# Kernel tuning notes

Measured on AMD Instinct MI355X. Metric: run time of the kernel, lower is better.

The kernel has to match this reference:

```python
import jax, jax.numpy as jnp
import numpy as np

B, S, D, H = 2, 2048, 1024, 16
HD = D // H  # 64
EPS = 1e-6


def setup_inputs() -> dict:
    key = jax.random.key(0)
    ks = jax.random.split(key, 12)
    s = 1.0 / np.sqrt(D)
    return {
        "query": jax.random.normal(ks[0], (B, S, D), jnp.float32),
        "key": jax.random.normal(ks[1], (B, S, D), jnp.float32),
        "value": jax.random.normal(ks[2], (B, S, D), jnp.float32),
        "mask": jax.random.randint(ks[3], (B, S, S), 0, 2) == 1,
        "Wq": jax.random.normal(ks[4], (D, D), jnp.float32) * s,
        "bq": jnp.zeros((D,), jnp.float32),
        "Wk": jax.random.normal(ks[5], (D, D), jnp.float32) * s,
        "bk": jnp.zeros((D,), jnp.float32),
        "Wv": jax.random.normal(ks[6], (D, D), jnp.float32) * s,
        "bv": jnp.zeros((D,), jnp.float32),
        "Wo": jax.random.normal(ks[7], (D, D), jnp.float32) * s,
        "bo": jnp.zeros((D,), jnp.float32),
        "gamma": jnp.ones((D,), jnp.float32),
        "beta": jnp.zeros((D,), jnp.float32),
    }


def reference(query, key, value, mask, Wq, bq, Wk, bk, Wv, bv, Wo, bo, gamma, beta):
    b, sq, _ = query.shape
    sk = key.shape[1]
    # QKV projections -> [b, h, s, hd]
    q = (query @ Wq + bq).reshape(b, sq, H, HD).transpose(0, 2, 1, 3)
    k = (key @ Wk + bk).reshape(b, sk, H, HD).transpose(0, 2, 1, 3)
    v = (value @ Wv + bv).reshape(b, sk, H, HD).transpose(0, 2, 1, 3)
    # scores [b, h, sq, sk]
    scores = jnp.einsum("bhqd,bhkd->bhqk", q, k) / jnp.sqrt(jnp.float32(HD))
    scores = jnp.where(mask[:, None, :, :], -jnp.inf, scores)
    attn = jax.nn.softmax(scores, axis=-1)  # dropout: eval mode (identity)
    out = jnp.einsum("bhqk,bhkd->bhqd", attn, v)
    out = out.transpose(0, 2, 1, 3).reshape(b, sq, H * HD)
    out = out @ Wo + bo
    # residual + LayerNorm with unbiased std and (std + eps) denominator (faithful to torch code)
    x = query + out
    mean = x.mean(-1, keepdims=True)
    std = jnp.std(x, axis=-1, keepdims=True, ddof=1)
    return gamma * (x - mean) / (std + EPS) + beta
```

## Files before the change

### kernel.cpp

```cpp
#include <hip/hip_runtime.h>


#define NB 2
#define SS 2048
#define DDIM 1024
#define NH 16
#define HDIM 64
#define MROWS (NB * SS)

typedef unsigned short u16;
typedef unsigned long long u64;
typedef unsigned int u32;
typedef short bf16x8 __attribute__((ext_vector_type(8)));
typedef float f32x4 __attribute__((ext_vector_type(4)));

typedef const __attribute__((address_space(1))) void GASV;
typedef __attribute__((address_space(3))) void LASV;

__device__ __forceinline__ float dev_exp2(float x) {
  float r;
  asm("v_exp_f32 %0, %1" : "=v"(r) : "v"(x));
  return r;
}

__device__ __forceinline__ u16 f2bf(float f) {
  unsigned u = __builtin_bit_cast(unsigned, f);
  u += 0x7FFFu + ((u >> 16) & 1u);
  return (u16)(u >> 16);
}

__device__ __forceinline__ u32 cvt_pk_bf16(float a, float b) {
  u32 d;
  asm("v_cvt_pk_bf16_f32 %0, %1, %2" : "=v"(d) : "v"(a), "v"(b));
  return d;
}

__global__ __launch_bounds__(256) void cvt_bf16_3(const float* __restrict__ q,
                                                  const float* __restrict__ k,
                                                  const float* __restrict__ v,
                                                  u16* __restrict__ out) {
  const float* in = (blockIdx.y == 0) ? q : (blockIdx.y == 1) ? k : v;
  size_t i = ((size_t)blockIdx.x * 256 + threadIdx.x) * 4;
  float4 val = *(const float4*)(in + i);
  uint2 o;
  u16* po = (u16*)&o;
  po[0] = f2bf(val.x); po[1] = f2bf(val.y); po[2] = f2bf(val.z); po[3] = f2bf(val.w);
  *(uint2*)(out + (size_t)blockIdx.y * MROWS * DDIM + i) = o;
}

__global__ __launch_bounds__(256) void cvt_mask_bits(const int* __restrict__ in,
                                                     u64* __restrict__ out) {
  size_t w = ((size_t)blockIdx.x * 256 + threadIdx.x) >> 6;
  int lane = threadIdx.x & 63;
  int v = in[w * 64 + lane];
  u64 bits = __ballot(v != 0);
  if (lane == 0) out[w] = bits;
}

__global__ __launch_bounds__(256) void transpose_cvt_w4(const float* __restrict__ W0,
                                                        const float* __restrict__ W1,
                                                        const float* __restrict__ W2,
                                                        const float* __restrict__ W3,
                                                        u16* __restrict__ WTbase) {
  __shared__ u16 t[64][65];
  const int z = blockIdx.z;
  const float* W = (z == 0) ? W0 : (z == 1) ? W1 : (z == 2) ? W2 : W3;
  u16* WT = WTbase + (size_t)z * DDIM * DDIM;
  const int k0 = blockIdx.x * 64, n0 = blockIdx.y * 64;
  const int tid = threadIdx.x;
  const int r = tid >> 4;
  const int c4 = (tid & 15) * 4;
#pragma unroll
  for (int it = 0; it < 4; ++it) {
    int k = r + it * 16;
    float4 v = *(const float4*)&W[(size_t)(k0 + k) * DDIM + n0 + c4];
    t[c4 + 0][k] = f2bf(v.x);
    t[c4 + 1][k] = f2bf(v.y);
    t[c4 + 2][k] = f2bf(v.z);
    t[c4 + 3][k] = f2bf(v.w);
  }
  __syncthreads();
#pragma unroll
  for (int it = 0; it < 4; ++it) {
    int n = r + it * 16;
    uint2 o;
    u16* po = (u16*)&o;
#pragma unroll
    for (int j = 0; j < 4; ++j) po[j] = t[n][c4 + j];
    *(uint2*)&WT[(size_t)(n0 + n) * DDIM + k0 + c4] = o;
  }
}

template <int MODE>
__global__ __launch_bounds__(256) void gemm_bt(const u16* __restrict__ Abase,
                                               const u16* __restrict__ BT,
                                               const float* __restrict__ b0,
                                               const float* __restrict__ b1,
                                               const float* __restrict__ b2,
                                               const float* __restrict__ resid,
                                               void* __restrict__ C,
                                               void* __restrict__ Cv) {
  __shared__ __align__(16) u16 SMEM[2][2][128][64];
  u16(&Al)[2][128][64] = SMEM[0];
  u16(&Bl)[2][128][64] = SMEM[1];
  const int tid = threadIdx.x;
  const int wid = tid >> 6, lane = tid & 63;
  const int wm = (wid >> 1) * 64, wn = (wid & 1) * 64;
  const int nwg = gridDim.x * gridDim.y;
  const int lin = blockIdx.y * 32 + blockIdx.x;
  const int wg = (lin & 7) * (nwg >> 3) + (lin >> 3);
  const int rowA0 = (wg & 31) * 128, colB0 = (wg >> 5) * 128;
  const int sel = (MODE == 0) ? (colB0 >> 10) : 0;
  const u16* Ag = Abase + (size_t)sel * ((size_t)MROWS * DDIM) + (size_t)rowA0 * DDIM;
  const u16* Bg = BT + (size_t)colB0 * DDIM;
  f32x4 acc[4][4] = {};
  const int rl = lane >> 3;
  const int ce = (lane & 7) * 8;

#define G_STAGE(buf, kt)                                                       \
  do {                                                                         \
    _Pragma("unroll") for (int c = 0; c < 4; ++c) {                            \
      int rt = wid * 32 + c * 8;                                               \
      __builtin_amdgcn_global_load_lds(                                        \
          (GASV*)(Ag + (size_t)(rt + rl) * DDIM + (kt) + ce),                  \
          (LASV*)((char*)&Al[buf][0][0] + rt * 128), 16, 0, 0);                \
      __builtin_amdgcn_global_load_lds(                                        \
          (GASV*)(Bg + (size_t)(rt + rl) * DDIM + (kt) + ce),                  \
          (LASV*)((char*)&Bl[buf][0][0] + rt * 128), 16, 0, 0);                \
    }                                                                          \
  } while (0)

  G_STAGE(0, 0);
  __syncthreads();
  for (int t = 0; t < 16; ++t) {
    const int cur = t & 1;
    if (t < 15) G_STAGE(cur ^ 1, (t + 1) * 64);
#pragma unroll
    for (int kk = 0; kk < 64; kk += 32) {
      bf16x8 af[4], bfr[4];
#pragma unroll
      for (int i = 0; i < 4; ++i)
        af[i] = *(const bf16x8*)&Al[cur][wm + i * 16 + (lane & 15)][kk + (lane >> 4) * 8];
#pragma unroll
      for (int j = 0; j < 4; ++j)
        bfr[j] = *(const bf16x8*)&Bl[cur][wn + j * 16 + (lane & 15)][kk + (lane >> 4) * 8];
#pragma unroll
      for (int i = 0; i < 4; ++i)
#pragma unroll
        for (int j = 0; j < 4; ++j)
          acc[i][j] = __builtin_amdgcn_mfma_f32_16x16x32_bf16(af[i], bfr[j], acc[i][j], 0, 0, 0);
    }
    __syncthreads();
  }
#undef G_STAGE

  const int cb = lane & 15, hi = lane >> 4;
  if (MODE == 0) {
    if (sel == 2) {
      u16(*T)[136] = (u16(*)[136]) & SMEM[0][0][0][0];
      const int dcol0 = colB0 & 1023;
#pragma unroll
      for (int j = 0; j < 4; ++j) {
        int dl = wn + j * 16 + cb;
        float bv = b2[dcol0 + dl];
#pragma unroll
        for (int i = 0; i < 4; ++i) {
          int sl = wm + i * 16 + hi * 4;
          uint2 o;
          o.x = cvt_pk_bf16(acc[i][j][0] + bv, acc[i][j][1] + bv);
          o.y = cvt_pk_bf16(acc[i][j][2] + bv, acc[i][j][3] + bv);
          *(uint2*)&T[dl][sl] = o;
        }
      }
      __syncthreads();
      const int bb = rowA0 >> 11, s0 = rowA0 & (SS - 1);
#pragma unroll
      for (int it = 0; it < 8; ++it) {
        int chunk = it * 256 + tid;
        int dl = chunk >> 4;
        int sc = (chunk & 15) * 8;
        int dg = dcol0 + dl;
        *(bf16x8*)&((u16*)Cv)[((size_t)(bb * NH + (dg >> 6)) * HDIM + (dg & 63)) * SS +
                              s0 + sc] = *(const bf16x8*)&T[dl][sc];
      }
    } else {
      const float* bp = (sel == 0) ? b0 : b1;
      const float scale = (sel == 0) ? 0.125f * 1.44269504088896340736f : 1.0f;
      u16* dst = (u16*)C + (size_t)sel * ((size_t)MROWS * DDIM);
      const int colw0 = (colB0 & 1023) + wn;
#pragma unroll
      for (int i = 0; i < 4; ++i)
#pragma unroll
        for (int j = 0; j < 4; ++j) {
          int colw = colw0 + j * 16 + cb;
          float bv = bp[colw];
#pragma unroll
          for (int r = 0; r < 4; ++r) {
            int row = rowA0 + wm + i * 16 + hi * 4 + r;
            dst[(size_t)row * DDIM + colw] = f2bf((acc[i][j][r] + bv) * scale);
          }
        }
    }
  } else {
#pragma unroll
    for (int i = 0; i < 4; ++i)
#pragma unroll
      for (int j = 0; j < 4; ++j) {
        int col = colB0 + wn + j * 16 + cb;
        float bv = b0[col];
#pragma unroll
        for (int r = 0; r < 4; ++r) {
          int row = rowA0 + wm + i * 16 + hi * 4 + r;
          size_t off = (size_t)row * DDIM + col;
          ((float*)C)[off] = acc[i][j][r] + bv + resid[off];
        }
      }
  }
}

__global__ __launch_bounds__(256, 4) void attn_fwd(const u16* __restrict__ Qp,
                                                   const u16* __restrict__ Kp,
                                                   const u16* __restrict__ VpT,
                                                   const u64* __restrict__ Mbits,
                                                   u16* __restrict__ O) {
  __shared__ __align__(16) u16 Kl[2][64][64];
  __shared__ __align__(16) u16 Vl[2][64][64];
  __shared__ __align__(16) u16 Pl[4][16][64];
  const int tid = threadIdx.x, wid = tid >> 6, lane = tid & 63;
  const int bid = blockIdx.x;
  const int bh = (bid & 7) * 4 + ((bid >> 3) & 3);
  const int q0 = (bid >> 5) * 64;
  const int b = bh >> 4, h = bh & 15;
  const int hi = lane >> 4, cbase = lane & 15, lx = lane & 7;

  bf16x8 qf[2];
  {
    const u16* qb = Qp + (size_t)(b * SS + q0 + wid * 16 + cbase) * DDIM + h * 64 + hi * 8;
    qf[0] = *(const bf16x8*)qb;
    qf[1] = *(const bf16x8*)(qb + 32);
  }
  const bf16x8 ONES8 = {(short)0x3F80, (short)0x3F80, (short)0x3F80, (short)0x3F80,
                        (short)0x3F80, (short)0x3F80, (short)0x3F80, (short)0x3F80};
  f32x4 l_acc = (f32x4){0.f, 0.f, 0.f, 0.f};
  f32x4 accO[4];
#pragma unroll
  for (int f = 0; f < 4; ++f) accO[f] = (f32x4){0.f, 0.f, 0.f, 0.f};

  const u16* Kgb = Kp + (size_t)b * SS * DDIM + h * 64;
  const u16* Vgb = VpT + (size_t)bh * 64 * SS;
  const u64* Mb = Mbits + (size_t)(b * SS + q0 + wid * 16 + cbase) * (SS / 64);
  const int rl = lane >> 3;
  const int ceS = ((lane & 7) ^ rl) * 8;

  int fo[4][2];
#pragma unroll
  for (int f = 0; f < 4; ++f)
#pragma unroll
    for (int ks = 0; ks < 2; ++ks)
      fo[f][ks] = (f * 16 + cbase) * 64 + (((ks * 4 + hi) ^ lx) << 3);
  int pw[4];
#pragma unroll
  for (int f = 0; f < 4; ++f)
    pw[f] = cbase * 64 + (((f * 2 + (hi >> 1)) ^ lx) << 3) + ((hi & 1) << 2);
  u16* KlF = &Kl[0][0][0];
  u16* VlF = &Vl[0][0][0];
  u16* Plw = &Pl[wid][0][0];

#define STAGE_KV(BUF, kv)                                                      \
  do {                                                                         \
    _Pragma("unroll") for (int c = 0; c < 2; ++c) {                            \
      int rt = wid * 16 + c * 8;                                               \
      __builtin_amdgcn_global_load_lds(                                        \
          (GASV*)(Kgb + (size_t)((kv) + rt + rl) * DDIM + ceS),                \
          (LASV*)((char*)KlF + (BUF) * 8192 + rt * 128), 16, 0, 0);            \
      __builtin_amdgcn_global_load_lds(                                        \
          (GASV*)(Vgb + (size_t)(rt + rl) * SS + (kv) + ceS),                  \
          (LASV*)((char*)VlF + (BUF) * 8192 + rt * 128), 16, 0, 0);            \
    }                                                                          \
  } while (0)

#define ATTN_ITER(T, CUR, DO_STAGE, MROW)                                      \
  do {                                                                         \
    if (DO_STAGE) STAGE_KV((CUR) ^ 1, ((T) + 1) * 64);                         \
    f32x4 sc[4];                                                               \
    __builtin_amdgcn_s_setprio(1);                                             \
    _Pragma("unroll") for (int fn = 0; fn < 4; ++fn) {                         \
      f32x4 c = (f32x4){0.f, 0.f, 0.f, 0.f};                                   \
      _Pragma("unroll") for (int ks = 0; ks < 2; ++ks) {                       \
        bf16x8 kf = *(const bf16x8*)(KlF + (CUR) * 4096 + fo[fn][ks]);         \
        c = __builtin_amdgcn_mfma_f32_16x16x32_bf16(kf, qf[ks], c, 0, 0, 0);   \
      }                                                                        \
      sc[fn] = c;                                                              \
    }                                                                          \
    __builtin_amdgcn_s_setprio(0);                                             \
             \
    u64 mh = (MROW) >> (hi * 4);                                               \
    u32 mlo = (u32)mh, mhi2 = (u32)(mh >> 32);                                 \
    _Pragma("unroll") for (int fn = 0; fn < 4; ++fn) {                         \
      u32 b4 = ((fn < 2) ? mlo : mhi2) >> ((fn & 1) * 16);                     \
      _Pragma("unroll") for (int j = 0; j < 4; ++j) {                          \
        float bf_ = (float)((b4 >> j) & 1u);                                   \
        sc[fn][j] = dev_exp2(fmaf(bf_, -512.f, sc[fn][j]));                    \
      }                                                                        \
    }                                                                          \
    _Pragma("unroll") for (int fn = 0; fn < 4; ++fn) {                         \
      uint2 wpair;                                                             \
      wpair.x = cvt_pk_bf16(sc[fn][0], sc[fn][1]);                             \
      wpair.y = cvt_pk_bf16(sc[fn][2], sc[fn][3]);                             \
      *(uint2*)(Plw + pw[fn]) = wpair;                                         \
    }                                                                          \
    bf16x8 pf0 = *(const bf16x8*)(Plw + fo[0][0]);                             \
    bf16x8 pf1 = *(const bf16x8*)(Plw + fo[0][1]);                             \
    __builtin_amdgcn_s_setprio(1);                                             \
    l_acc = __builtin_amdgcn_mfma_f32_16x16x32_bf16(pf0, ONES8, l_acc, 0, 0, 0); \
    l_acc = __builtin_amdgcn_mfma_f32_16x16x32_bf16(pf1, ONES8, l_acc, 0, 0, 0); \
    _Pragma("unroll") for (int nd = 0; nd < 4; ++nd) {                         \
      bf16x8 v0 = *(const bf16x8*)(VlF + (CUR) * 4096 + fo[nd][0]);            \
      bf16x8 v1 = *(const bf16x8*)(VlF + (CUR) * 4096 + fo[nd][1]);            \
      accO[nd] = __builtin_amdgcn_mfma_f32_16x16x32_bf16(pf0, v0, accO[nd], 0, 0, 0); \
      accO[nd] = __builtin_amdgcn_mfma_f32_16x16x32_bf16(pf1, v1, accO[nd], 0, 0, 0); \
    }                                                                          \
    __builtin_amdgcn_s_setprio(0);                                             \
    __syncthreads();                                                           \
  } while (0)

  STAGE_KV(0, 0);
  __syncthreads();
  for (int th = 0; th < 16; ++th) {
    uint4 mw = *(const uint4*)&Mb[2 * th];
    u64 m0 = ((u64)mw.y << 32) | mw.x;
    u64 m1 = ((u64)mw.w << 32) | mw.z;
    ATTN_ITER(2 * th, 0, true, m0);
    ATTN_ITER(2 * th + 1, 1, (th != 15), m1);
  }
#undef ATTN_ITER
#undef STAGE_KV

#pragma unroll
  for (int nd = 0; nd < 4; ++nd)
#pragma unroll
    for (int j = 0; j < 4; ++j) {
      int row = q0 + wid * 16 + hi * 4 + j;
      int col = h * 64 + nd * 16 + cbase;
      O[(size_t)(b * SS + row) * DDIM + col] = f2bf(accO[nd][j] / l_acc[j]);
    }
}

__global__ __launch_bounds__(256) void ln_res(const float* __restrict__ xin,
                                              const float* __restrict__ gamma,
                                              const float* __restrict__ beta,
                                              float* __restrict__ out) {
  const int row = blockIdx.x, tid = threadIdx.x;
  const size_t base = (size_t)row * DDIM + tid * 4;
  float4 x = *(const float4*)(xin + base);
  float x0 = x.x, x1 = x.y, x2 = x.z, x3 = x.w;
  float s = x0 + x1 + x2 + x3;
  __shared__ float red[4];
#pragma unroll
  for (int off = 32; off >= 1; off >>= 1) s += __shfl_xor(s, off, 64);
  const int wid = tid >> 6, lane = tid & 63;
  if (lane == 0) red[wid] = s;
  __syncthreads();
  float mean = (red[0] + red[1] + red[2] + red[3]) * (1.0f / DDIM);
  float d0 = x0 - mean, d1 = x1 - mean, d2 = x2 - mean, d3 = x3 - mean;
  float ss = d0 * d0 + d1 * d1 + d2 * d2 + d3 * d3;
#pragma unroll
  for (int off = 32; off >= 1; off >>= 1) ss += __shfl_xor(ss, off, 64);
  __syncthreads();
  if (lane == 0) red[wid] = ss;
  __syncthreads();
  float var = (red[0] + red[1] + red[2] + red[3]) * (1.0f / (DDIM - 1));
  float denom = sqrtf(var) + 1e-6f;
  float4 g = *(const float4*)(gamma + (size_t)tid * 4);
  float4 be = *(const float4*)(beta + (size_t)tid * 4);
  float4 o;
  o.x = g.x * d0 / denom + be.x;
  o.y = g.y * d1 / denom + be.y;
  o.z = g.z * d2 / denom + be.z;
  o.w = g.w * d3 / denom + be.w;
  *(float4*)(out + base) = o;
}

extern "C" void kernel_launch(void* const* d_in, const int* in_sizes, int n_in,
                              void* d_out, int out_size, void* d_ws, size_t ws_size,
                              hipStream_t stream) {
  const float* query = (const float*)d_in[0];
  const float* key = (const float*)d_in[1];
  const float* value = (const float*)d_in[2];
  const int* mask = (const int*)d_in[3];
  const float* Wq = (const float*)d_in[4];
  const float* bq = (const float*)d_in[5];
  const float* Wk = (const float*)d_in[6];
  const float* bk = (const float*)d_in[7];
  const float* Wv = (const float*)d_in[8];
  const float* bv = (const float*)d_in[9];
  const float* Wo = (const float*)d_in[10];
  const float* bo = (const float*)d_in[11];
  const float* gamma = (const float*)d_in[12];
  const float* beta = (const float*)d_in[13];
  float* out = (float*)d_out;
  char* ws = (char*)d_ws;
  const size_t MB = 1ull << 20;
  u16* qkvb = (u16*)(ws + 0 * MB);
  u16* WT = (u16*)(ws + 24 * MB);
  u16* WoT = (u16*)(ws + 30 * MB);
  u16* Qp = (u16*)(ws + 32 * MB);
  u16* Kp = (u16*)(ws + 40 * MB);
  u16* VpT = (u16*)(ws + 48 * MB);
  u16* attnb = (u16*)(ws + 56 * MB);
  u64* maskbits = (u64*)(ws + 0 * MB);
  float* proj = (float*)(ws + 8 * MB);

  cvt_bf16_3<<<dim3(MROWS * DDIM / 1024, 3), 256, 0, stream>>>(query, key, value, qkvb);
  transpose_cvt_w4<<<dim3(16, 16, 4), 256, 0, stream>>>(Wq, Wk, Wv, Wo, WT);
  gemm_bt<0><<<dim3(32, 24), 256, 0, stream>>>(qkvb, WT, bq, bk, bv, nullptr, Qp, VpT);
  cvt_mask_bits<<<(NB * SS * SS) / 256, 256, 0, stream>>>(mask, maskbits);
  attn_fwd<<<1024, 256, 0, stream>>>(Qp, Kp, VpT, maskbits, attnb);
  gemm_bt<1><<<dim3(32, 8), 256, 0, stream>>>(attnb, WoT, bo, nullptr, nullptr,
                                              query, proj, nullptr);
  ln_res<<<MROWS, 256, 0, stream>>>(proj, gamma, beta, out);
}
```

Baseline: 158.2 us.

## Enlarge attention tile to 128 queries, remap GEMM tiles per XCD, wave-per-row LayerNorm

The attention kernel now runs 512 threads (8 waves) per block covering 128 query rows. Each staged K/V tile is therefore shared by twice as many waves, and each wave issues half as many loads. The GEMM workgroup-to-tile mapping now gives each XCD a contiguous set of row blocks across all column tiles, which should improve L2 reuse of A. LayerNorm now uses one wavefront per row with shuffle-only reductions, dropping the shared-memory syncs, and multiplies by a reciprocal instead of dividing. The larger attention block may reduce occupancy, and the mixed changes make attribution harder.

```diff
diff --git a/kernel.cpp b/kernel.cpp
--- a/kernel.cpp
+++ b/kernel.cpp
@@ -106,10 +106,11 @@
   const int tid = threadIdx.x;
   const int wid = tid >> 6, lane = tid & 63;
   const int wm = (wid >> 1) * 64, wn = (wid & 1) * 64;
-  const int nwg = gridDim.x * gridDim.y;
+  const int NCOL = (MODE == 0) ? 24 : 8;
   const int lin = blockIdx.y * 32 + blockIdx.x;
-  const int wg = (lin & 7) * (nwg >> 3) + (lin >> 3);
-  const int rowA0 = (wg & 31) * 128, colB0 = (wg >> 5) * 128;
+  const int xcd = lin & 7, idx = lin >> 3;
+  const int rowA0 = (xcd * 4 + idx / NCOL) * 128;
+  const int colB0 = (idx % NCOL) * 128;
   const int sel = (MODE == 0) ? (colB0 >> 10) : 0;
   const u16* Ag = Abase + (size_t)sel * ((size_t)MROWS * DDIM) + (size_t)rowA0 * DDIM;
   const u16* Bg = BT + (size_t)colB0 * DDIM;
@@ -218,18 +219,18 @@
   }
 }
 
-__global__ __launch_bounds__(256, 4) void attn_fwd(const u16* __restrict__ Qp,
+__global__ __launch_bounds__(512, 6) void attn_fwd(const u16* __restrict__ Qp,
                                                    const u16* __restrict__ Kp,
                                                    const u16* __restrict__ VpT,
                                                    const u64* __restrict__ Mbits,
                                                    u16* __restrict__ O) {
   __shared__ __align__(16) u16 Kl[2][64][64];
   __shared__ __align__(16) u16 Vl[2][64][64];
-  __shared__ __align__(16) u16 Pl[4][16][64];
+  __shared__ __align__(16) u16 Pl[8][16][64];
   const int tid = threadIdx.x, wid = tid >> 6, lane = tid & 63;
   const int bid = blockIdx.x;
   const int bh = (bid & 7) * 4 + ((bid >> 3) & 3);
-  const int q0 = (bid >> 5) * 64;
+  const int q0 = (bid >> 5) * 128;
   const int b = bh >> 4, h = bh & 15;
   const int hi = lane >> 4, cbase = lane & 15, lx = lane & 7;
 
@@ -268,15 +269,13 @@
 
 #define STAGE_KV(BUF, kv)                                                      \
   do {                                                                         \
-    _Pragma("unroll") for (int c = 0; c < 2; ++c) {                            \
-      int rt = wid * 16 + c * 8;                                               \
-      __builtin_amdgcn_global_load_lds(                                        \
-          (GASV*)(Kgb + (size_t)((kv) + rt + rl) * DDIM + ceS),                \
-          (LASV*)((char*)KlF + (BUF) * 8192 + rt * 128), 16, 0, 0);            \
-      __builtin_amdgcn_global_load_lds(                                        \
-          (GASV*)(Vgb + (size_t)(rt + rl) * SS + (kv) + ceS),                  \
-          (LASV*)((char*)VlF + (BUF) * 8192 + rt * 128), 16, 0, 0);            \
-    }                                                                          \
+    int rt = wid * 8;                                                          \
+    __builtin_amdgcn_global_load_lds(                                          \
+        (GASV*)(Kgb + (size_t)((kv) + rt + rl) * DDIM + ceS),                  \
+        (LASV*)((char*)KlF + (BUF) * 8192 + rt * 128), 16, 0, 0);              \
+    __builtin_amdgcn_global_load_lds(                                          \
+        (GASV*)(Vgb + (size_t)(rt + rl) * SS + (kv) + ceS),                    \
+        (LASV*)((char*)VlF + (BUF) * 8192 + rt * 128), 16, 0, 0);              \
   } while (0)
 
 #define ATTN_ITER(T, CUR, DO_STAGE, MROW)                                      \
@@ -350,35 +349,41 @@
                                               const float* __restrict__ gamma,
                                               const float* __restrict__ beta,
                                               float* __restrict__ out) {
-  const int row = blockIdx.x, tid = threadIdx.x;
-  const size_t base = (size_t)row * DDIM + tid * 4;
-  float4 x = *(const float4*)(xin + base);
-  float x0 = x.x, x1 = x.y, x2 = x.z, x3 = x.w;
-  float s = x0 + x1 + x2 + x3;
-  __shared__ float red[4];
+  const int tid = threadIdx.x, wid = tid >> 6, lane = tid & 63;
+  const int row = blockIdx.x * 4 + wid;
+  const float* xr = xin + (size_t)row * DDIM;
+  float4 x[4];
+  float s = 0.f;
+#pragma unroll
+  for (int i = 0; i < 4; ++i) {
+    x[i] = *(const float4*)(xr + lane * 4 + i * 256);
+    s += (x[i].x + x[i].y) + (x[i].z + x[i].w);
+  }
 #pragma unroll
   for (int off = 32; off >= 1; off >>= 1) s += __shfl_xor(s, off, 64);
-  const int wid = tid >> 6, lane = tid & 63;
-  if (lane == 0) red[wid] = s;
-  __syncthreads();
-  float mean = (red[0] + red[1] + red[2] + red[3]) * (1.0f / DDIM);
-  float d0 = x0 - mean, d1 = x1 - mean, d2 = x2 - mean, d3 = x3 - mean;
-  float ss = d0 * d0 + d1 * d1 + d2 * d2 + d3 * d3;
+  float mean = s * (1.0f / DDIM);
+  float ss = 0.f;
+#pragma unroll
+  for (int i = 0; i < 4; ++i) {
+    x[i].x -= mean; x[i].y -= mean; x[i].z -= mean; x[i].w -= mean;
+    ss += (x[i].x * x[i].x + x[i].y * x[i].y) + (x[i].z * x[i].z + x[i].w * x[i].w);
+  }
 #pragma unroll
   for (int off = 32; off >= 1; off >>= 1) ss += __shfl_xor(ss, off, 64);
-  __syncthreads();
-  if (lane == 0) red[wid] = ss;
-  __syncthreads();
-  float var = (red[0] + red[1] + red[2] + red[3]) * (1.0f / (DDIM - 1));
-  float denom = sqrtf(var) + 1e-6f;
-  float4 g = *(const float4*)(gamma + (size_t)tid * 4);
-  float4 be = *(const float4*)(beta + (size_t)tid * 4);
-  float4 o;
-  o.x = g.x * d0 / denom + be.x;
-  o.y = g.y * d1 / denom + be.y;
-  o.z = g.z * d2 / denom + be.z;
-  o.w = g.w * d3 / denom + be.w;
-  *(float4*)(out + base) = o;
+  float var = ss * (1.0f / (DDIM - 1));
+  float rden = 1.0f / (sqrtf(var) + 1e-6f);
+  float* orow = out + (size_t)row * DDIM;
+#pragma unroll
+  for (int i = 0; i < 4; ++i) {
+    float4 g = *(const float4*)(gamma + lane * 4 + i * 256);
+    float4 be = *(const float4*)(beta + lane * 4 + i * 256);
+    float4 o;
+    o.x = g.x * x[i].x * rden + be.x;
+    o.y = g.y * x[i].y * rden + be.y;
+    o.z = g.z * x[i].z * rden + be.z;
+    o.w = g.w * x[i].w * rden + be.w;
+    *(float4*)(orow + lane * 4 + i * 256) = o;
+  }
 }
 
 extern "C" void kernel_launch(void* const* d_in, const int* in_sizes, int n_in,
@@ -415,8 +420,8 @@
   transpose_cvt_w4<<<dim3(16, 16, 4), 256, 0, stream>>>(Wq, Wk, Wv, Wo, WT);
   gemm_bt<0><<<dim3(32, 24), 256, 0, stream>>>(qkvb, WT, bq, bk, bv, nullptr, Qp, VpT);
   cvt_mask_bits<<<(NB * SS * SS) / 256, 256, 0, stream>>>(mask, maskbits);
-  attn_fwd<<<1024, 256, 0, stream>>>(Qp, Kp, VpT, maskbits, attnb);
+  attn_fwd<<<512, 512, 0, stream>>>(Qp, Kp, VpT, maskbits, attnb);
   gemm_bt<1><<<dim3(32, 8), 256, 0, stream>>>(attnb, WoT, bo, nullptr, nullptr,
                                               query, proj, nullptr);
-  ln_res<<<MROWS, 256, 0, stream>>>(proj, gamma, beta, out);
-}
+  ln_res<<<MROWS / 4, 256, 0, stream>>>(proj, gamma, beta, out);
+}
```

Result: no change. 155.8 us (-1.6%).
